# Kernel tuning notes

Measured on AMD Instinct MI355X. Metric: run time of the kernel, lower is better.

The kernel has to match this reference:

```python
import jax, jax.numpy as jnp
import numpy as np

R = 32          # voxel_resolution
GN_GROUPS = 8   # GroupNorm groups used throughout the module


def group_norm(x, scale, bias, groups, eps=1e-5):
    B, C = x.shape[0], x.shape[1]
    spatial = x.shape[2:]
    xg = x.reshape(B, groups, C // groups, -1)
    mu = xg.mean(axis=(2, 3), keepdims=True)
    var = xg.var(axis=(2, 3), keepdims=True)
    xn = ((xg - mu) / jnp.sqrt(var + eps)).reshape((B, C) + spatial)
    sh = (1, C) + (1,) * len(spatial)
    return xn * scale.reshape(sh) + bias.reshape(sh)


def conv3d_same(x, w, b):
    pad = w.shape[-1] // 2
    y = jax.lax.conv_general_dilated(
        x, w, (1, 1, 1), [(pad, pad)] * 3,
        dimension_numbers=('NCDHW', 'OIDHW', 'NCDHW'))
    return y + b.reshape(1, -1, 1, 1, 1)


def _voxelize(coords, features, r):
    # PVCNN Voxelization: center coords, normalize to [0,1], scale to grid,
    # scatter-MEAN point features into a dense [B,C,r,r,r] grid.
    B, C, N = features.shape
    centered = coords - coords.mean(axis=2, keepdims=True)            # [B,3,N]
    norm = jnp.linalg.norm(centered, axis=1, keepdims=True)           # [B,1,N]
    denom = norm.max(axis=2, keepdims=True) * 2.0                     # eps = 0
    nc = centered / denom + 0.5
    nc = jnp.clip(nc * r, 0.0, r - 1.0)                               # float voxel coords
    vi = jnp.round(nc).astype(jnp.int32)                              # [B,3,N]
    flat = (vi[:, 0] * r + vi[:, 1]) * r + vi[:, 2]                   # [B,N]
    seg = (flat + (jnp.arange(B, dtype=jnp.int32) * (r ** 3))[:, None]).reshape(-1)
    feats = features.transpose(0, 2, 1).reshape(B * N, C)
    sums = jax.ops.segment_sum(feats, seg, num_segments=B * r ** 3)
    cnts = jax.ops.segment_sum(jnp.ones((B * N,), feats.dtype), seg,
                               num_segments=B * r ** 3)
    mean = sums / jnp.maximum(cnts, 1.0)[:, None]
    grid = mean.reshape(B, r, r, r, C).transpose(0, 4, 1, 2, 3)       # [B,C,r,r,r]
    return nc, grid


def _trilinear_devoxelize(nc, grid, r):
    # nc [B,3,N] float in [0,r-1]; grid [B,C,r,r,r] -> gather 8 corners + weights
    B, C = grid.shape[0], grid.shape[1]
    lo = jnp.floor(nc)
    frac = nc - lo                                                    # [B,3,N]
    lo_i = lo.astype(jnp.int32)
    hi_i = jnp.minimum(lo_i + 1, r - 1)
    gf = grid.reshape(B, C, r * r * r)
    out = jnp.zeros((B, C, nc.shape[2]), grid.dtype)
    for dx in (0, 1):
        for dy in (0, 1):
            for dz in (0, 1):
                ix = hi_i[:, 0] if dx else lo_i[:, 0]
                iy = hi_i[:, 1] if dy else lo_i[:, 1]
                iz = hi_i[:, 2] if dz else lo_i[:, 2]
                w = ((frac[:, 0] if dx else 1.0 - frac[:, 0]) *
                     (frac[:, 1] if dy else 1.0 - frac[:, 1]) *
                     (frac[:, 2] if dz else 1.0 - frac[:, 2]))        # [B,N]
                idx = (ix * r + iy) * r + iz                          # [B,N]
                g = jnp.take_along_axis(gf, idx[:, None, :], axis=2)  # [B,C,N]
                out = out + g * w[:, None, :]
    return out


def setup_inputs() -> dict:
    key = jax.random.key(0)
    ks = jax.random.split(key, 6)
    B, N, Cin, Cout, K = 4, 65536, 64, 128, 3
    return {
        'coords':   jax.random.normal(ks[0], (B, 3, N), jnp.float32),
        'features': jax.random.normal(ks[1], (B, Cin, N), jnp.float32),
        'conv1_w':  jax.random.normal(ks[2], (Cout, Cin, K, K, K), jnp.float32) * 0.02,
        'conv1_b':  jnp.zeros((Cout,), jnp.float32),
        'gn1_scale': jnp.ones((Cout,), jnp.float32),
        'gn1_bias':  jnp.zeros((Cout,), jnp.float32),
        'conv2_w':  jax.random.normal(ks[3], (Cout, Cout, K, K, K), jnp.float32) * 0.02,
        'conv2_b':  jnp.zeros((Cout,), jnp.float32),
        'gn2_scale': jnp.ones((Cout,), jnp.float32),
        'gn2_bias':  jnp.zeros((Cout,), jnp.float32),
        'point_w':  jax.random.normal(ks[4], (Cout, Cin), jnp.float32) * 0.05,
        'point_b':  jnp.zeros((Cout,), jnp.float32),
        'point_gn_scale': jnp.ones((Cout,), jnp.float32),
        'point_gn_bias':  jnp.zeros((Cout,), jnp.float32),
    }


def reference(coords, features, conv1_w, conv1_b, gn1_scale, gn1_bias,
              conv2_w, conv2_b, gn2_scale, gn2_bias,
              point_w, point_b, point_gn_scale, point_gn_bias):
    nc, grid = _voxelize(coords, features, R)
    # voxel branch: Conv3d -> GN -> SiLU -> (dropout, eval: identity) -> Conv3d -> GN -> SiLU
    h = conv3d_same(grid, conv1_w, conv1_b)
    h = jax.nn.silu(group_norm(h, gn1_scale, gn1_bias, GN_GROUPS))
    h = conv3d_same(h, conv2_w, conv2_b)
    h = jax.nn.silu(group_norm(h, gn2_scale, gn2_bias, GN_GROUPS))
    # point branch: SharedMLP = 1x1 Conv1d -> GN -> SiLU
    p = jnp.einsum('oc,bcn->bon', point_w, features) + point_b[None, :, None]
    p = jax.nn.silu(group_norm(p, point_gn_scale, point_gn_bias, GN_GROUPS))
    vpts = _trilinear_devoxelize(nc, h, R)                            # [B,Cout,N]
    return p + vpts
```

## Files before the change

kernel.cpp:

```cpp
#include <hip/hip_runtime.h>

typedef __attribute__((ext_vector_type(8))) short bf16x8;
typedef __attribute__((ext_vector_type(4))) float f32x4;
typedef __attribute__((ext_vector_type(4))) int i32x4;
typedef __attribute__((ext_vector_type(2))) int i32x2;

#define B_ 4
#define N_ 65536
#define RRR_ 32768
#define PADV_ 39304
#define PPLANE_ 1156

static const size_t OFF_NC     = 0;
static const size_t OFF_VIDX   = 786432;
static const size_t OFF_WT1    = 1048576;
static const size_t OFF_WT2    = 1159168;
static const size_t OFF_C2OUT  = 1380352;
static const size_t OFF_CNT    = 9768960;
static const size_t OFF_GSUM   = 9900032;
static const size_t OFF_GPAD   = 18288640;
static const size_t OFF_ACT1   = 23319552;
static const size_t OFF_GSTATS = 33381376;
static const size_t OFF_BSTATS = 33381568;
static const size_t MEMSET_FLOATS = 33381584 - 9768960;
static const size_t OFF_PBF    = 9900032;

__device__ __forceinline__ ushort f2bf(float x) {
    union { float f; unsigned u; } c; c.f = x;
    unsigned r = c.u + 0x7fffu + ((c.u >> 16) & 1u);
    return (ushort)(r >> 16);
}
__device__ __forceinline__ float bf2f(ushort h) {
    union { unsigned u; float f; } c; c.u = ((unsigned)h) << 16;
    return c.f;
}

__device__ __forceinline__ void gl16(const void* g, void* l) {
    __builtin_amdgcn_global_load_lds(
        (const __attribute__((address_space(1))) unsigned int*)(g),
        (__attribute__((address_space(3))) unsigned int*)(l),
        16, 0, 0);
}

__global__ __launch_bounds__(256) void k_coord_sum(const float* __restrict__ coords,
                                                   float* __restrict__ bstats) {
    int b = blockIdx.y;
    int tid = threadIdx.x;
    const float* cb = coords + (size_t)b * 3 * N_;
    float s0 = 0.f, s1 = 0.f, s2 = 0.f;
    for (int n = blockIdx.x * 256 + tid; n < N_; n += 64 * 256) {
        s0 += cb[n]; s1 += cb[N_ + n]; s2 += cb[2 * N_ + n];
    }
    #pragma unroll
    for (int off = 1; off < 64; off <<= 1) {
        s0 += __shfl_xor(s0, off);
        s1 += __shfl_xor(s1, off);
        s2 += __shfl_xor(s2, off);
    }
    if ((tid & 63) == 0) {
        atomicAdd(&bstats[b * 4 + 0], s0);
        atomicAdd(&bstats[b * 4 + 1], s1);
        atomicAdd(&bstats[b * 4 + 2], s2);
    }
}

__global__ __launch_bounds__(256) void k_coord_max(const float* __restrict__ coords,
                                                   float* __restrict__ bstats) {
    int b = blockIdx.y;
    int tid = threadIdx.x;
    const float invN = 1.0f / (float)N_;
    float m0 = bstats[b * 4 + 0] * invN;
    float m1 = bstats[b * 4 + 1] * invN;
    float m2 = bstats[b * 4 + 2] * invN;
    const float* cb = coords + (size_t)b * 3 * N_;
    float mx = 0.f;
    for (int n = blockIdx.x * 256 + tid; n < N_; n += 64 * 256) {
        float x = cb[n] - m0, y = cb[N_ + n] - m1, z = cb[2 * N_ + n] - m2;
        mx = fmaxf(mx, x * x + y * y + z * z);
    }
    #pragma unroll
    for (int off = 1; off < 64; off <<= 1)
        mx = fmaxf(mx, __shfl_xor(mx, off));
    if ((tid & 63) == 0)
        atomicMax((int*)&bstats[b * 4 + 3], __float_as_int(mx));
}

__global__ __launch_bounds__(256) void k_point_prep(const float* __restrict__ coords,
                                                    const float* __restrict__ bstats,
                                                    float* __restrict__ nc,
                                                    int* __restrict__ vidx,
                                                    float* __restrict__ cnt) {
    int gid = blockIdx.x * 256 + threadIdx.x;
    int b = gid >> 16;
    int n = gid & (N_ - 1);
    const float invN = 1.0f / (float)N_;
    float m[3] = {bstats[b * 4 + 0] * invN, bstats[b * 4 + 1] * invN, bstats[b * 4 + 2] * invN};
    float den = 2.0f * sqrtf(__int_as_float(((const int*)bstats)[b * 4 + 3]));
    const float* cb = coords + (size_t)b * 3 * N_;
    int vi[3];
    #pragma unroll
    for (int d = 0; d < 3; ++d) {
        float cv = cb[(size_t)d * N_ + n];
        float t = (cv - m[d]) / den + 0.5f;
        t *= 32.0f;
        t = fminf(fmaxf(t, 0.0f), 31.0f);
        nc[((size_t)b * 3 + d) * N_ + n] = t;
        vi[d] = (int)rintf(t);
    }
    int flat = (vi[0] * 32 + vi[1]) * 32 + vi[2];
    vidx[(b << 16) + n] = flat;
    atomicAdd(&cnt[(b << 15) + flat], 1.0f);
}

__global__ __launch_bounds__(256) void k_scatter_cl(const float* __restrict__ feats,
                                                    const int* __restrict__ vidx,
                                                    float* __restrict__ gsum) {
    __shared__ float lf[64 * 129];
    __shared__ int sidx[128];
    int tid = threadIdx.x;
    int b = blockIdx.y;
    int n0 = blockIdx.x * 128;
    for (int i = tid; i < 64 * 128; i += 256) {
        int ci = i >> 7, pt = i & 127;
        lf[ci * 129 + pt] = feats[((size_t)(b * 64 + ci)) * N_ + n0 + pt];
    }
    if (tid < 128) sidx[tid] = vidx[(b << 16) + n0 + tid];
    __syncthreads();
    for (int i = tid; i < 64 * 128; i += 256) {
        int ci = i & 63, pt = i >> 6;
        atomicAdd(&gsum[((size_t)(b << 15) + sidx[pt]) * 64 + ci], lf[ci * 129 + pt]);
    }
}

__global__ __launch_bounds__(256) void k_gridmean_cl(const float* __restrict__ gsum,
                                                     const float* __restrict__ cnt,
                                                     ushort* __restrict__ gpad) {
    int idx = blockIdx.x * 256 + threadIdx.x;
    int q = idx & 15;
    int vox = (idx >> 4) & 32767;
    int b = idx >> 19;
    float c = cnt[(b << 15) + vox];
    float inv = 1.0f / fmaxf(c, 1.0f);
    float4 v = *(const float4*)(gsum + (((size_t)(b << 15) + vox) << 6) + q * 4);
    int zz = vox >> 10, yy = (vox >> 5) & 31, xx = vox & 31;
    size_t o = ((size_t)b * PADV_ + (size_t)(zz + 1) * PPLANE_ + (yy + 1) * 34 + (xx + 1)) * 64 + q * 4;
    i32x2 pk;
    ushort* u = (ushort*)&pk;
    u[0] = f2bf(v.x * inv); u[1] = f2bf(v.y * inv);
    u[2] = f2bf(v.z * inv); u[3] = f2bf(v.w * inv);
    *(i32x2*)(gpad + o) = pk;
}

template <int CI>
__global__ __launch_bounds__(256) void k_wtrans(const float* __restrict__ w,
                                                ushort* __restrict__ wt) {
    int idx = blockIdx.x * 256 + threadIdx.x;
    if (idx >= 27 * 128 * CI) return;
    int e = idx & 7;
    int jm = (idx >> 3) & 7;
    int co = (idx >> 6) & 127;
    int ks = idx >> 13;
    int q = jm ^ (co & 7);
    int tap = (CI == 64) ? ks : (ks >> 1);
    int ci = ((CI == 64) ? 0 : ((ks & 1) * 64)) + q * 8 + e;
    wt[idx] = f2bf(w[((size_t)co * CI + ci) * 27 + tap]);
}

template <int CI, bool PAD_OUT>
__global__ __launch_bounds__(256, 2) void k_conv(const ushort* __restrict__ inp,
                                                 const ushort* __restrict__ wt,
                                                 const float* __restrict__ bias,
                                                 ushort* __restrict__ outp,
                                                 float* __restrict__ gstats,
                                                 int layer) {
    constexpr int NK = 27 * CI / 64;
    __shared__ char lds[65536];

    const int bid = blockIdx.x;
    const int wid = (bid & 7) * 128 + (bid >> 3);
    const int yg = wid & 7;
    const int z0 = (wid >> 3) & 31;
    const int b = wid >> 8;
    const int y0 = yg * 4;
    const int tid = threadIdx.x;
    const int w = tid >> 6, l = tid & 63;
    const int lk = l >> 4, lr = l & 15;
    const int wr = w >> 1, wc = w & 1;

    const char* actb = (const char*)(inp + (size_t)b * PADV_ * CI);
    const char* wtb = (const char*)wt;

    const char* agp[4];
    #pragma unroll
    for (int i = 0; i < 4; ++i) {
        int s = tid + i * 256;
        int row = s >> 3, j = s & 7;
        int jj = j ^ (row & 7);
        int py = row >> 5, px = row & 31;
        agp[i] = actb + ((size_t)(z0 * PPLANE_ + (y0 + py) * 34 + px) * CI) * 2 + jj * 16;
    }

    int ard[4][2], brd[4][2];
    #pragma unroll
    for (int i = 0; i < 4; ++i) {
        int pos = wr * 64 + i * 16 + lr;
        #pragma unroll
        for (int kk = 0; kk < 2; ++kk)
            ard[i][kk] = pos * 128 + (((kk * 4 + lk) ^ (pos & 7)) << 4);
    }
    #pragma unroll
    for (int n = 0; n < 4; ++n) {
        int co = wc * 64 + n * 16 + lr;
        #pragma unroll
        for (int kk = 0; kk < 2; ++kk)
            brd[n][kk] = 16384 + co * 128 + (((kk * 4 + lk) ^ (co & 7)) << 4);
    }

    f32x4 acc[4][4];
    #pragma unroll
    for (int i = 0; i < 4; ++i)
        #pragma unroll
        for (int n = 0; n < 4; ++n)
            acc[i][n] = (f32x4){0.f, 0.f, 0.f, 0.f};

    auto stage = [&](int ks, int cur) {
        int tap = (CI == 64) ? ks : (ks >> 1);
        int choff2 = (CI == 64) ? 0 : ((ks & 1) << 7);
        int fz = tap / 9, r9 = tap - fz * 9;
        int fy = r9 / 3, fx = r9 - fy * 3;
        int ad = (fz * PPLANE_ + fy * 34 + fx) * CI * 2 + choff2;
        char* base = lds + cur * 32768;
        #pragma unroll
        for (int i = 0; i < 4; ++i)
            gl16(agp[i] + ad, base + w * 1024 + i * 4096);
        const char* wsrc = wtb + (size_t)ks * 16384 + tid * 16;
        #pragma unroll
        for (int i = 0; i < 4; ++i)
            gl16(wsrc + i * 4096, base + 16384 + w * 1024 + i * 4096);
    };

    stage(0, 0);

    #pragma unroll 1
    for (int ks = 0; ks < NK; ++ks) {
        const int cur = ks & 1;
        if (ks + 1 < NK) {
            stage(ks + 1, cur ^ 1);
            __builtin_amdgcn_sched_barrier(0);
            asm volatile("s_waitcnt vmcnt(8)" ::: "memory");
            __builtin_amdgcn_sched_barrier(0);
        } else {
            __builtin_amdgcn_sched_barrier(0);
            asm volatile("s_waitcnt vmcnt(0)" ::: "memory");
            __builtin_amdgcn_sched_barrier(0);
        }
        __builtin_amdgcn_s_barrier();
        __builtin_amdgcn_sched_barrier(0);
        const char* Ac = lds + cur * 32768;
        __builtin_amdgcn_s_setprio(1);
        #pragma unroll
        for (int kk = 0; kk < 2; ++kk) {
            bf16x8 af[4], bfr[4];
            #pragma unroll
            for (int i = 0; i < 4; ++i) af[i] = *(const bf16x8*)(Ac + ard[i][kk]);
            #pragma unroll
            for (int n = 0; n < 4; ++n) bfr[n] = *(const bf16x8*)(Ac + brd[n][kk]);
            #pragma unroll
            for (int i = 0; i < 4; ++i)
                #pragma unroll
                for (int n = 0; n < 4; ++n)
                    acc[i][n] = __builtin_amdgcn_mfma_f32_16x16x32_bf16(af[i], bfr[n], acc[i][n], 0, 0, 0);
        }
        __builtin_amdgcn_s_setprio(0);
        __builtin_amdgcn_sched_barrier(0);
        __builtin_amdgcn_s_barrier();
        __builtin_amdgcn_sched_barrier(0);
    }

    __syncthreads();
    ushort* outs = (ushort*)lds;
    float bb[4];
    #pragma unroll
    for (int n = 0; n < 4; ++n) bb[n] = bias[wc * 64 + n * 16 + lr];
    float sg[4] = {0.f, 0.f, 0.f, 0.f}, sq[4] = {0.f, 0.f, 0.f, 0.f};
    #pragma unroll
    for (int i = 0; i < 4; ++i) {
        int posb = wr * 64 + i * 16 + lk * 4;
        #pragma unroll
        for (int n = 0; n < 4; ++n) {
            int co = wc * 64 + n * 16 + lr;
            #pragma unroll
            for (int r = 0; r < 4; ++r) {
                float v = acc[i][n][r] + bb[n];
                sg[n] += v; sq[n] += v * v;
                outs[(posb + r) * 128 + co] = f2bf(v);
            }
        }
    }
    #pragma unroll
    for (int off = 1; off < 64; off <<= 1) {
        #pragma unroll
        for (int n = 0; n < 4; ++n) {
            sg[n] += __shfl_xor(sg[n], off);
            sq[n] += __shfl_xor(sq[n], off);
        }
    }
    if (l == 0) {
        int gbase = layer * 32 + b * 8 + wc * 4;
        #pragma unroll
        for (int n = 0; n < 4; ++n) {
            atomicAdd(&gstats[(gbase + n) * 2 + 0], sg[n]);
            atomicAdd(&gstats[(gbase + n) * 2 + 1], sq[n]);
        }
    }
    __syncthreads();
    for (int idx = tid; idx < 2048; idx += 256) {
        int pos = idx >> 4, c8 = idx & 15;
        int yy = y0 + (pos >> 5), xx = pos & 31;
        size_t g;
        if (PAD_OUT)
            g = ((size_t)b * PADV_ + (size_t)(z0 + 1) * PPLANE_ + (yy + 1) * 34 + (xx + 1)) * 128 + c8 * 8;
        else
            g = ((size_t)b * RRR_ + z0 * 1024 + yy * 32 + xx) * 128 + c8 * 8;
        *(i32x4*)(outp + g) = *((i32x4*)lds + idx);
    }
}

template <bool PAD>
__global__ __launch_bounds__(256) void k_gn_apply(ushort* __restrict__ x,
                                                  const float* __restrict__ gstats,
                                                  const float* __restrict__ sc,
                                                  const float* __restrict__ bi,
                                                  int layer, float invc) {
    int idx = blockIdx.x * 256 + threadIdx.x;
    int c8 = idx & 15;
    int vox = (idx >> 4) & 32767;
    int b = idx >> 19;
    size_t base;
    if (PAD) {
        int zz = vox >> 10, yy = (vox >> 5) & 31, xx = vox & 31;
        base = ((size_t)b * PADV_ + (size_t)(zz + 1) * PPLANE_ + (yy + 1) * 34 + (xx + 1)) * 128 + c8 * 8;
    } else {
        base = ((size_t)b * RRR_ + vox) * 128 + c8 * 8;
    }
    int g = c8 >> 1;
    float sum = gstats[(layer * 32 + b * 8 + g) * 2 + 0];
    float ssq = gstats[(layer * 32 + b * 8 + g) * 2 + 1];
    float mean = sum * invc;
    float var = ssq * invc - mean * mean;
    float rstd = rsqrtf(var + 1e-5f);
    i32x4 raw = *(i32x4*)(x + base);
    ushort* u = (ushort*)&raw;
    #pragma unroll
    for (int j = 0; j < 8; ++j) {
        int co = c8 * 8 + j;
        float v = bf2f(u[j]);
        v = (v - mean) * rstd * sc[co] + bi[co];
        v = v / (1.f + __expf(-v));
        u[j] = f2bf(v);
    }
    *(i32x4*)(x + base) = raw;
}

__global__ __launch_bounds__(256) void k_point_mlp(const float* __restrict__ feats,
                                                   const float* __restrict__ w,
                                                   const float* __restrict__ pb,
                                                   ushort* __restrict__ pbf,
                                                   float* __restrict__ gstats) {
    __shared__ float wl[64 * 132];
    __shared__ float sred[4][16];
    int tid = threadIdx.x;
    for (int i = tid; i < 128 * 64; i += 256) {
        int o = i >> 6, c = i & 63;
        wl[c * 132 + o] = w[i];
    }
    __syncthreads();
    int gid = blockIdx.x * 256 + tid;
    int b = gid >> 16, n = gid & (N_ - 1);
    const float* fb = feats + (size_t)b * 64 * N_ + n;
    float acc[128];
    #pragma unroll
    for (int o = 0; o < 128; ++o) acc[o] = 0.f;
    for (int c = 0; c < 64; ++c) {
        float f = fb[(size_t)c * N_];
        const float4* wr4 = (const float4*)&wl[c * 132];
        #pragma unroll
        for (int o4 = 0; o4 < 32; ++o4) {
            float4 wv = wr4[o4];
            acc[4 * o4 + 0] = fmaf(f, wv.x, acc[4 * o4 + 0]);
            acc[4 * o4 + 1] = fmaf(f, wv.y, acc[4 * o4 + 1]);
            acc[4 * o4 + 2] = fmaf(f, wv.z, acc[4 * o4 + 2]);
            acc[4 * o4 + 3] = fmaf(f, wv.w, acc[4 * o4 + 3]);
        }
    }
    ushort* ob = pbf + (size_t)b * 128 * N_ + n;
    float sg[8] = {0.f}, sq[8] = {0.f};
    #pragma unroll
    for (int o = 0; o < 128; ++o) {
        float v = acc[o] + pb[o];
        ob[(size_t)o * N_] = f2bf(v);
        sg[o >> 4] += v;
        sq[o >> 4] += v * v;
    }
    #pragma unroll
    for (int off = 1; off < 64; off <<= 1) {
        #pragma unroll
        for (int g = 0; g < 8; ++g) {
            sg[g] += __shfl_xor(sg[g], off);
            sq[g] += __shfl_xor(sq[g], off);
        }
    }
    int wv = tid >> 6, l = tid & 63;
    if (l == 0) {
        #pragma unroll
        for (int g = 0; g < 8; ++g) { sred[wv][g] = sg[g]; sred[wv][8 + g] = sq[g]; }
    }
    __syncthreads();
    if (tid < 16) {
        float v = sred[0][tid] + sred[1][tid] + sred[2][tid] + sred[3][tid];
        int g = tid & 7, part = tid >> 3;
        atomicAdd(&gstats[(64 + b * 8 + g) * 2 + part], v);
    }
}

__global__ __launch_bounds__(256) void k_devox_final(const float* __restrict__ nc,
                                                     const ushort* __restrict__ ht,
                                                     const ushort* __restrict__ pbf,
                                                     const float* __restrict__ gstats,
                                                     const float* __restrict__ scale,
                                                     const float* __restrict__ bias,
                                                     float* __restrict__ out) {
    __shared__ float vp[64][129];
    __shared__ int sidx[64][8];
    __shared__ float swt[64][8];
    int tid = threadIdx.x;
    int blk = blockIdx.x;
    int b = blk >> 10;
    int n0 = (blk & 1023) * 64;
    if (tid < 64) {
        int n = n0 + tid;
        float f0 = nc[(size_t)b * 3 * N_ + n];
        float f1 = nc[((size_t)b * 3 + 1) * N_ + n];
        float f2 = nc[((size_t)b * 3 + 2) * N_ + n];
        float l0 = floorf(f0), l1 = floorf(f1), l2 = floorf(f2);
        float r0 = f0 - l0, r1 = f1 - l1, r2 = f2 - l2;
        int i0 = (int)l0, i1 = (int)l1, i2 = (int)l2;
        int h0 = min(i0 + 1, 31), h1 = min(i1 + 1, 31), h2 = min(i2 + 1, 31);
        #pragma unroll
        for (int k = 0; k < 8; ++k) {
            int dx = (k >> 2) & 1, dy = (k >> 1) & 1, dz = k & 1;
            int ix = dx ? h0 : i0, iy = dy ? h1 : i1, iz = dz ? h2 : i2;
            float w = (dx ? r0 : 1.f - r0) * (dy ? r1 : 1.f - r1) * (dz ? r2 : 1.f - r2);
            sidx[tid][k] = (ix * 32 + iy) * 32 + iz;
            swt[tid][k] = w;
        }
    }
    __syncthreads();
    const ushort* hb = ht + (size_t)b * RRR_ * 128;
    for (int t = tid; t < 64 * 16; t += 256) {
        int c8 = t & 15, pt = t >> 4;
        float a[8] = {0.f, 0.f, 0.f, 0.f, 0.f, 0.f, 0.f, 0.f};
        #pragma unroll
        for (int k = 0; k < 8; ++k) {
            i32x4 raw = *(const i32x4*)(hb + (size_t)sidx[pt][k] * 128 + c8 * 8);
            ushort* u = (ushort*)&raw;
            float wk = swt[pt][k];
            #pragma unroll
            for (int j = 0; j < 8; ++j)
                a[j] = fmaf(wk, bf2f(u[j]), a[j]);
        }
        #pragma unroll
        for (int j = 0; j < 8; ++j)
            vp[pt][c8 * 8 + j] = a[j];
    }
    __syncthreads();
    const float invc = 1.0f / (16.0f * (float)N_);
    for (int t = tid; t < 64 * 128; t += 256) {
        int nl = t & 63;
        int c = t >> 6;
        int g = c >> 4;
        float sum = gstats[(64 + b * 8 + g) * 2 + 0];
        float ssq = gstats[(64 + b * 8 + g) * 2 + 1];
        float mean = sum * invc;
        float var = ssq * invc - mean * mean;
        float rstd = rsqrtf(var + 1e-5f);
        size_t o = ((size_t)(b * 128 + c)) * N_ + n0 + nl;
        float v = (bf2f(pbf[o]) - mean) * rstd * scale[c] + bias[c];
        v = v / (1.f + __expf(-v));
        out[o] = v + vp[nl][c];
    }
}

extern "C" void kernel_launch(void* const* d_in, const int* in_sizes, int n_in,
                              void* d_out, int out_size, void* d_ws, size_t ws_size,
                              hipStream_t stream) {
    const float* coords   = (const float*)d_in[0];
    const float* features = (const float*)d_in[1];
    const float* conv1_w  = (const float*)d_in[2];
    const float* conv1_b  = (const float*)d_in[3];
    const float* gn1_s    = (const float*)d_in[4];
    const float* gn1_b    = (const float*)d_in[5];
    const float* conv2_w  = (const float*)d_in[6];
    const float* conv2_b  = (const float*)d_in[7];
    const float* gn2_s    = (const float*)d_in[8];
    const float* gn2_b    = (const float*)d_in[9];
    const float* point_w  = (const float*)d_in[10];
    const float* point_b  = (const float*)d_in[11];
    const float* pgn_s    = (const float*)d_in[12];
    const float* pgn_b    = (const float*)d_in[13];
    float* out = (float*)d_out;
    float* ws = (float*)d_ws;

    float*  nc     = ws + OFF_NC;
    int*    vidx   = (int*)(ws + OFF_VIDX);
    ushort* wt1    = (ushort*)(ws + OFF_WT1);
    ushort* wt2    = (ushort*)(ws + OFF_WT2);
    ushort* c2out  = (ushort*)(ws + OFF_C2OUT);
    float*  cnt    = ws + OFF_CNT;
    float*  gsum   = ws + OFF_GSUM;
    ushort* gpad   = (ushort*)(ws + OFF_GPAD);
    ushort* act1   = (ushort*)(ws + OFF_ACT1);
    float*  gstats = ws + OFF_GSTATS;
    float*  bstats = ws + OFF_BSTATS;
    ushort* pbf    = (ushort*)(ws + OFF_PBF);

    const float invc = 1.0f / (float)(RRR_ * 16);

    hipMemsetAsync(cnt, 0, MEMSET_FLOATS * sizeof(float), stream);

    k_coord_sum<<<dim3(64, B_), 256, 0, stream>>>(coords, bstats);
    k_coord_max<<<dim3(64, B_), 256, 0, stream>>>(coords, bstats);
    k_point_prep<<<B_ * N_ / 256, 256, 0, stream>>>(coords, bstats, nc, vidx, cnt);
    k_scatter_cl<<<dim3(N_ / 128, B_), 256, 0, stream>>>(features, vidx, gsum);
    k_gridmean_cl<<<B_ * RRR_ * 16 / 256, 256, 0, stream>>>(gsum, cnt, gpad);

    k_wtrans<64><<<(27 * 128 * 64 + 255) / 256, 256, 0, stream>>>(conv1_w, wt1);
    k_wtrans<128><<<(27 * 128 * 128 + 255) / 256, 256, 0, stream>>>(conv2_w, wt2);

    k_conv<64, true><<<1024, 256, 0, stream>>>(gpad, wt1, conv1_b, act1, gstats, 0);
    k_gn_apply<true><<<B_ * RRR_ * 16 / 256, 256, 0, stream>>>(act1, gstats, gn1_s, gn1_b, 0, invc);

    k_conv<128, false><<<1024, 256, 0, stream>>>(act1, wt2, conv2_b, c2out, gstats, 1);
    k_gn_apply<false><<<B_ * RRR_ * 16 / 256, 256, 0, stream>>>(c2out, gstats, gn2_s, gn2_b, 1, invc);

    k_point_mlp<<<B_ * N_ / 256, 256, 0, stream>>>(features, point_w, point_b, pbf, gstats);
    k_devox_final<<<B_ * N_ / 64, 256, 0, stream>>>(nc, c2out, pbf, gstats, pgn_s, pgn_b, out);
}
```

Baseline: 936.5 us.

## Rewrite point MLP with bf16 MFMA tiles and remap devox block order

Replaces the scalar FP32 per-point 1x1 conv with a tiled kernel. Each block loads 128 points by 64 channels of features plus the weights into swizzled LDS as bf16, computes with 16x16x32 bf16 MFMA, and stages the output through LDS for coalesced 16-byte stores. It also remaps the block index in the devoxelize kernel so consecutive blocks interleave across batches and positions. The weights and features are now rounded to bf16 before the matmul, which lowers accuracy relative to the FP32 FMA path.

```diff
diff --git a/kernel.cpp b/kernel.cpp
--- a/kernel.cpp
+++ b/kernel.cpp
@@ -362,64 +362,116 @@
     *(i32x4*)(x + base) = raw;
 }
 
-__global__ __launch_bounds__(256) void k_point_mlp(const float* __restrict__ feats,
-                                                   const float* __restrict__ w,
-                                                   const float* __restrict__ pb,
-                                                   ushort* __restrict__ pbf,
-                                                   float* __restrict__ gstats) {
-    __shared__ float wl[64 * 132];
-    __shared__ float sred[4][16];
-    int tid = threadIdx.x;
-    for (int i = tid; i < 128 * 64; i += 256) {
-        int o = i >> 6, c = i & 63;
-        wl[c * 132 + o] = w[i];
-    }
-    __syncthreads();
-    int gid = blockIdx.x * 256 + tid;
-    int b = gid >> 16, n = gid & (N_ - 1);
-    const float* fb = feats + (size_t)b * 64 * N_ + n;
-    float acc[128];
-    #pragma unroll
-    for (int o = 0; o < 128; ++o) acc[o] = 0.f;
-    for (int c = 0; c < 64; ++c) {
-        float f = fb[(size_t)c * N_];
-        const float4* wr4 = (const float4*)&wl[c * 132];
-        #pragma unroll
-        for (int o4 = 0; o4 < 32; ++o4) {
-            float4 wv = wr4[o4];
-            acc[4 * o4 + 0] = fmaf(f, wv.x, acc[4 * o4 + 0]);
-            acc[4 * o4 + 1] = fmaf(f, wv.y, acc[4 * o4 + 1]);
-            acc[4 * o4 + 2] = fmaf(f, wv.z, acc[4 * o4 + 2]);
-            acc[4 * o4 + 3] = fmaf(f, wv.w, acc[4 * o4 + 3]);
-        }
-    }
-    ushort* ob = pbf + (size_t)b * 128 * N_ + n;
-    float sg[8] = {0.f}, sq[8] = {0.f};
-    #pragma unroll
-    for (int o = 0; o < 128; ++o) {
-        float v = acc[o] + pb[o];
-        ob[(size_t)o * N_] = f2bf(v);
-        sg[o >> 4] += v;
-        sq[o >> 4] += v * v;
+__global__ __launch_bounds__(256, 2) void k_point_mlp_mfma(const float* __restrict__ feats,
+                                                           const float* __restrict__ w,
+                                                           const float* __restrict__ pb,
+                                                           ushort* __restrict__ pbf,
+                                                           float* __restrict__ gstats) {
+    __shared__ char lds[32768];
+    const int bid = blockIdx.x;
+    const int b = bid >> 9;
+    const int n0 = (bid & 511) * 128;
+    const int tid = threadIdx.x;
+    const int wv = tid >> 6, l = tid & 63;
+    const int lk = l >> 4, lr = l & 15;
+    const int wr = wv >> 1, wc = wv & 1;
+
+    const float* fb = feats + (size_t)b * 64 * N_ + n0;
+    #pragma unroll
+    for (int it = 0; it < 8; ++it) {
+        int s = tid + it * 256;
+        int pt = s & 127, chq = s >> 7;
+        float f0 = fb[(size_t)(chq * 4 + 0) * N_ + pt];
+        float f1 = fb[(size_t)(chq * 4 + 1) * N_ + pt];
+        float f2 = fb[(size_t)(chq * 4 + 2) * N_ + pt];
+        float f3 = fb[(size_t)(chq * 4 + 3) * N_ + pt];
+        i32x2 pk;
+        unsigned* up = (unsigned*)&pk;
+        up[0] = (unsigned)f2bf(f0) | ((unsigned)f2bf(f1) << 16);
+        up[1] = (unsigned)f2bf(f2) | ((unsigned)f2bf(f3) << 16);
+        *(i32x2*)(lds + pt * 128 + (((chq >> 1) ^ (pt & 7)) << 4) + (chq & 1) * 8) = pk;
+    }
+    #pragma unroll
+    for (int it = 0; it < 8; ++it) {
+        int s = tid + it * 256;
+        int ciq = s & 15, co = s >> 4;
+        const float* wr4 = w + co * 64 + ciq * 4;
+        i32x2 pk;
+        unsigned* up = (unsigned*)&pk;
+        up[0] = (unsigned)f2bf(wr4[0]) | ((unsigned)f2bf(wr4[1]) << 16);
+        up[1] = (unsigned)f2bf(wr4[2]) | ((unsigned)f2bf(wr4[3]) << 16);
+        *(i32x2*)(lds + 16384 + co * 128 + (((ciq >> 1) ^ (co & 7)) << 4) + (ciq & 1) * 8) = pk;
+    }
+    __syncthreads();
+
+    f32x4 acc[4][4];
+    #pragma unroll
+    for (int i = 0; i < 4; ++i)
+        #pragma unroll
+        for (int n = 0; n < 4; ++n)
+            acc[i][n] = (f32x4){0.f, 0.f, 0.f, 0.f};
+
+    #pragma unroll
+    for (int kk = 0; kk < 2; ++kk) {
+        bf16x8 af[4], bfr[4];
+        #pragma unroll
+        for (int i = 0; i < 4; ++i) {
+            int pt = wr * 64 + i * 16 + lr;
+            af[i] = *(const bf16x8*)(lds + pt * 128 + (((kk * 4 + lk) ^ (pt & 7)) << 4));
+        }
+        #pragma unroll
+        for (int n = 0; n < 4; ++n) {
+            int co = wc * 64 + n * 16 + lr;
+            bfr[n] = *(const bf16x8*)(lds + 16384 + co * 128 + (((kk * 4 + lk) ^ (co & 7)) << 4));
+        }
+        #pragma unroll
+        for (int i = 0; i < 4; ++i)
+            #pragma unroll
+            for (int n = 0; n < 4; ++n)
+                acc[i][n] = __builtin_amdgcn_mfma_f32_16x16x32_bf16(af[i], bfr[n], acc[i][n], 0, 0, 0);
+    }
+
+    __syncthreads();
+    float bb[4];
+    #pragma unroll
+    for (int n = 0; n < 4; ++n) bb[n] = pb[wc * 64 + n * 16 + lr];
+    float sg[4] = {0.f, 0.f, 0.f, 0.f}, sq[4] = {0.f, 0.f, 0.f, 0.f};
+    ushort* outs = (ushort*)lds;
+    #pragma unroll
+    for (int i = 0; i < 4; ++i) {
+        #pragma unroll
+        for (int n = 0; n < 4; ++n) {
+            int co = wc * 64 + n * 16 + lr;
+            #pragma unroll
+            for (int r = 0; r < 4; ++r) {
+                int pt = wr * 64 + i * 16 + lk * 4 + r;
+                float v = acc[i][n][r] + bb[n];
+                sg[n] += v; sq[n] += v * v;
+                outs[co * 128 + ((((pt >> 3) ^ (co & 15)) << 3) | (pt & 7))] = f2bf(v);
+            }
+        }
     }
     #pragma unroll
     for (int off = 1; off < 64; off <<= 1) {
         #pragma unroll
-        for (int g = 0; g < 8; ++g) {
-            sg[g] += __shfl_xor(sg[g], off);
-            sq[g] += __shfl_xor(sq[g], off);
-        }
-    }
-    int wv = tid >> 6, l = tid & 63;
+        for (int n = 0; n < 4; ++n) {
+            sg[n] += __shfl_xor(sg[n], off);
+            sq[n] += __shfl_xor(sq[n], off);
+        }
+    }
     if (l == 0) {
         #pragma unroll
-        for (int g = 0; g < 8; ++g) { sred[wv][g] = sg[g]; sred[wv][8 + g] = sq[g]; }
-    }
-    __syncthreads();
-    if (tid < 16) {
-        float v = sred[0][tid] + sred[1][tid] + sred[2][tid] + sred[3][tid];
-        int g = tid & 7, part = tid >> 3;
-        atomicAdd(&gstats[(64 + b * 8 + g) * 2 + part], v);
+        for (int n = 0; n < 4; ++n) {
+            int g = wc * 4 + n;
+            atomicAdd(&gstats[(64 + b * 8 + g) * 2 + 0], sg[n]);
+            atomicAdd(&gstats[(64 + b * 8 + g) * 2 + 1], sq[n]);
+        }
+    }
+    __syncthreads();
+    for (int idx = tid; idx < 2048; idx += 256) {
+        int co = idx >> 4, c16 = idx & 15;
+        i32x4 v = *(i32x4*)(lds + co * 256 + ((c16 ^ (co & 15)) << 4));
+        *(i32x4*)(pbf + ((size_t)(b * 128 + co)) * N_ + n0 + c16 * 8) = v;
     }
 }
 
@@ -435,8 +487,9 @@
     __shared__ float swt[64][8];
     int tid = threadIdx.x;
     int blk = blockIdx.x;
-    int b = blk >> 10;
-    int n0 = (blk & 1023) * 64;
+    int wid = (blk & 7) * 512 + (blk >> 3);
+    int b = wid >> 10;
+    int n0 = (wid & 1023) * 64;
     if (tid < 64) {
         int n = n0 + tid;
         float f0 = nc[(size_t)b * 3 * N_ + n];
@@ -543,6 +596,6 @@
     k_conv<128, false><<<1024, 256, 0, stream>>>(act1, wt2, conv2_b, c2out, gstats, 1);
     k_gn_apply<false><<<B_ * RRR_ * 16 / 256, 256, 0, stream>>>(c2out, gstats, gn2_s, gn2_b, 1, invc);
 
-    k_point_mlp<<<B_ * N_ / 256, 256, 0, stream>>>(features, point_w, point_b, pbf, gstats);
+    k_point_mlp_mfma<<<2048, 256, 0, stream>>>(features, point_w, point_b, pbf, gstats);
     k_devox_final<<<B_ * N_ / 64, 256, 0, stream>>>(nc, c2out, pbf, gstats, pgn_s, pgn_b, out);
 }
```

New measurement: 1.351 ms. 44.2% more time.
